# Kernel tuning notes

Measured on AMD Instinct MI355X. Metric: run time of the kernel, lower is better.

The kernel has to match this reference:

```python
import jax, jax.numpy as jnp
import numpy as np

EMBD_SIZE = 128
NUM_HEADS = 8
HEAD_SIZE = 16

def setup_inputs() -> dict:
    key = jax.random.key(0)
    ks = jax.random.split(key, 6)
    B, S = 8, 2048
    x = jax.random.normal(ks[0], (B, S, EMBD_SIZE), dtype=jnp.float32)
    # per-head Linear weights, torch layout [out, in] stacked over heads -> [H, hs, E]
    sc = 1.0 / np.sqrt(EMBD_SIZE)
    Wk = jax.random.normal(ks[1], (NUM_HEADS, HEAD_SIZE, EMBD_SIZE), dtype=jnp.float32) * sc
    Wq = jax.random.normal(ks[2], (NUM_HEADS, HEAD_SIZE, EMBD_SIZE), dtype=jnp.float32) * sc
    Wv = jax.random.normal(ks[3], (NUM_HEADS, HEAD_SIZE, EMBD_SIZE), dtype=jnp.float32) * sc
    Wp = jax.random.normal(ks[4], (EMBD_SIZE, NUM_HEADS * HEAD_SIZE), dtype=jnp.float32) * sc
    bp = jax.random.normal(ks[5], (EMBD_SIZE,), dtype=jnp.float32) * 0.01
    return {"x": x, "Wk": Wk, "Wq": Wq, "Wv": Wv, "Wp": Wp, "bp": bp}

def reference(x, Wk, Wq, Wv, Wp, bp):
    # x: [B,S,E]; W{k,q,v}: [H,hs,E]; Wp: [E,H*hs]
    B, S, E = x.shape
    H, hs, _ = Wk.shape
    q = jnp.einsum('bse,hde->bhsd', x, Wq)
    k = jnp.einsum('bse,hde->bhsd', x, Wk)
    v = jnp.einsum('bse,hde->bhsd', x, Wv)
    # NOTE: original code MULTIPLIES by sqrt(head_size) (k.shape[-1]**0.5)
    scores = jnp.einsum('bhsd,bhtd->bhst', q, k) * (hs ** 0.5)
    wei = jax.nn.softmax(scores, axis=-1)  # dropout is identity in eval mode
    out = jnp.einsum('bhst,bhtd->bhsd', wei, v)
    # concat heads along last dim: [B,S,H*hs]
    out = out.transpose(0, 2, 1, 3).reshape(B, S, H * hs)
    return out @ Wp.T + bp
```

## Files before the change

### kernel.cpp

```cpp
#include <hip/hip_runtime.h>
#include <hip/hip_bf16.h>

constexpr int Bb  = 8;
constexpr int Ss  = 2048;
constexpr int Ee  = 128;
constexpr int Hh  = 8;
constexpr int HSs = 16;
constexpr int QKVSZ = Bb * Hh * Ss * HSs;

typedef _Float16 f16;
typedef __attribute__((ext_vector_type(8)))  _Float16 f16x8;
typedef __attribute__((ext_vector_type(16))) float f32x16;

constexpr float QSCALE = 5.770780163555854f;

__device__ __forceinline__ unsigned pack_rtz(float lo, float hi) {
    union { __fp16 __attribute__((ext_vector_type(2))) h; unsigned u; } c;
    c.h = __builtin_amdgcn_cvt_pkrtz(lo, hi);
    return c.u;
}
__device__ __forceinline__ unsigned pack_rne(float lo, float hi) {
    union { __attribute__((ext_vector_type(2))) _Float16 h; unsigned u; } c;
    c.h[0] = (f16)lo; c.h[1] = (f16)hi;
    return c.u;
}

__device__ __forceinline__ float vmax16(const f32x16& v) {
    float a = fmaxf(fmaxf(v[0],  v[1]),  v[2]);
    float b = fmaxf(fmaxf(v[3],  v[4]),  v[5]);
    float c = fmaxf(fmaxf(v[6],  v[7]),  v[8]);
    float d = fmaxf(fmaxf(v[9],  v[10]), v[11]);
    float e = fmaxf(fmaxf(v[12], v[13]), v[14]);
    float g = fmaxf(fmaxf(a, b), c);
    float h = fmaxf(fmaxf(d, e), v[15]);
    return fmaxf(g, h);
}

__device__ __forceinline__ f16x8 cvt8(const float4& w0, const float4& w1) {
    union { f16x8 v; unsigned u[4]; } wf;
    wf.u[0] = pack_rne(w0.x, w0.y); wf.u[1] = pack_rne(w0.z, w0.w);
    wf.u[2] = pack_rne(w1.x, w1.y); wf.u[3] = pack_rne(w1.z, w1.w);
    return wf.v;
}

__global__ __launch_bounds__(256) void qkv_kernel(
    const float* __restrict__ x,
    const float* __restrict__ Wq, const float* __restrict__ Wk,
    const float* __restrict__ Wv,
    f16* __restrict__ qo, f16* __restrict__ ko, f16* __restrict__ vo)
{
    constexpr int LDW = 136;
    __shared__ __align__(16) f16 Xs[32 * LDW];

    const int rowbase = blockIdx.x * 32;

    for (int idx = threadIdx.x; idx < 32 * 32; idx += 256) {
        const int r = idx >> 5, cp = idx & 31;
        float4 v = *(const float4*)(x + (size_t)(rowbase + r) * Ee + cp * 4);
        union { f16 h[4]; uint2 u; } cv;
        cv.h[0] = (f16)v.x; cv.h[1] = (f16)v.y; cv.h[2] = (f16)v.z; cv.h[3] = (f16)v.w;
        *(uint2*)&Xs[r * LDW + cp * 4] = cv.u;
    }
    __syncthreads();

    const int wv_ = threadIdx.x >> 6, lane = threadIdx.x & 63;
    const int h = lane >> 5, n31 = lane & 31;

    f16x8 A[8];
#pragma unroll
    for (int t = 0; t < 8; ++t)
        A[t] = *(const f16x8*)&Xs[n31 * LDW + 16 * t + 8 * h];

    const int c = wv_ * 32 + n31;
    const int b = rowbase >> 11;
    const int s0 = rowbase & 2047;
    const int head = c >> 4, d = c & 15;
    const int bh = b * Hh + head;
    const int it = s0 >> 6, g0 = (s0 >> 4) & 3;

#pragma unroll
    for (int mat = 0; mat < 3; ++mat) {
        const float* W = (mat == 0) ? Wq : (mat == 1) ? Wk : Wv;
        const float* wr32 = W + (size_t)c * Ee + 8 * h;
        f32x16 acc = {};
#pragma unroll
        for (int t = 0; t < 8; ++t) {
            float4 w0 = *(const float4*)(wr32 + 16 * t);
            float4 w1 = *(const float4*)(wr32 + 16 * t + 4);
            acc = __builtin_amdgcn_mfma_f32_32x32x16_f16(A[t], cvt8(w0, w1), acc, 0, 0, 0);
        }

        if (mat < 2) {
            f16* dst = (mat == 0) ? qo : ko;
            const float scale = (mat == 1) ? QSCALE : 1.f;
#pragma unroll
            for (int r = 0; r < 16; ++r) {
                const int s = s0 + (r & 3) + 8 * (r >> 2) + 4 * h;
                dst[((size_t)bh * Ss + s) * HSs + d] = (f16)(acc[r] * scale);
            }
        } else {
            f16* vb = vo + (size_t)bh * 65536 + it * 2048;
#pragma unroll
            for (int rq = 0; rq < 4; ++rq) {
                union { f16 hv[4]; uint2 u; } pk4;
#pragma unroll
                for (int i = 0; i < 4; ++i) pk4.hv[i] = (f16)acc[4 * rq + i];
                *(uint2*)(vb + (g0 + (rq >> 1)) * 512 + (d + 32 * h) * 8 + 4 * (rq & 1)) = pk4.u;
            }
        }
    }

    for (int i = threadIdx.x; i < 512; i += 256) {
        const int gp = i >> 8, hd = (i >> 5) & 7, cc = i & 31;
        const int lanep = (cc < 16) ? 16 + cc : 32 + cc;
        const unsigned one2 = 0x3C003C00u;
        uint4 val = ((cc & 15) == 0) ? (uint4){one2, one2, one2, one2}
                                     : (uint4){0, 0, 0, 0};
        *(uint4*)(vo + (size_t)(b * Hh + hd) * 65536 + it * 2048
                  + (g0 + gp) * 512 + lanep * 8) = val;
    }
}

__global__ __launch_bounds__(512, 4) void attn_kernel(
    const f16* __restrict__ qg, const f16* __restrict__ kg,
    const f16* __restrict__ vg, const float* __restrict__ wp32,
    const float* __restrict__ bp, float* __restrict__ out)
{
    constexpr int LDW = 136;
    __shared__ __align__(16) f16 Os[32 * LDW];

    const int b    = blockIdx.x & 7;
    const int qblk = blockIdx.x >> 3;
    const int wid  = threadIdx.x >> 6;
    const int lane = threadIdx.x & 63;
    const int h    = lane >> 5;
    const int q31  = lane & 31;
    const int qbase = qblk * 32;
    const int bh   = b * Hh + wid;

    const f16x8 qf = *(const f16x8*)(qg + ((size_t)bh * Ss + qbase + q31) * HSs + 8 * h);

    const f16* pk = kg + (size_t)bh * Ss * HSs + q31 * 16 + 8 * h;
    const f16* pv = vg + (size_t)bh * 65536 + lane * 8;

    f16x8 ka0 = *(const f16x8*)pk;
    f16x8 ka1 = *(const f16x8*)(pk + 512);
    f16x8 va0 = *(const f16x8*)(pv);
    f16x8 va1 = *(const f16x8*)(pv + 512);
    f16x8 va2 = *(const f16x8*)(pv + 1024);
    f16x8 va3 = *(const f16x8*)(pv + 1536);

    f32x16 acc = {};
    f32x16 cinit = {};

    constexpr int NIT = Ss / 64;
    for (int it = 0; it < NIT; ++it) {
        f32x16 st0 = __builtin_amdgcn_mfma_f32_32x32x16_f16(ka0, qf, cinit, 0, 0, 0);
        f32x16 st1 = __builtin_amdgcn_mfma_f32_32x32x16_f16(ka1, qf, cinit, 0, 0, 0);

        if (it + 1 < NIT) {
            pk += 1024;
            ka0 = *(const f16x8*)pk;
            ka1 = *(const f16x8*)(pk + 512);
        }

        float mx = fmaxf(vmax16(st0), vmax16(st1));
        mx = fmaxf(mx, __shfl_xor(mx, 32, 64));

        if (__any(mx > 8.f)) {
            const float delta = fmaxf(mx, 0.f);
            const float corr  = __builtin_amdgcn_exp2f(-delta);
#pragma unroll
            for (int r = 0; r < 9; ++r) acc[r] *= corr;
#pragma unroll
            for (int t = 0; t < 16; ++t) { st0[t] -= delta; st1[t] -= delta; }
#pragma unroll
            for (int r = 0; r < 16; ++r) cinit[r] -= delta;
        }

        union { unsigned u[4]; f16x8 v; } B1, B2, B3, B4;
#pragma unroll
        for (int r = 0; r < 4; ++r) {
            B1.u[r] = pack_rtz(__builtin_amdgcn_exp2f(st0[2 * r]),
                               __builtin_amdgcn_exp2f(st0[2 * r + 1]));
            B2.u[r] = pack_rtz(__builtin_amdgcn_exp2f(st0[8 + 2 * r]),
                               __builtin_amdgcn_exp2f(st0[9 + 2 * r]));
            B3.u[r] = pack_rtz(__builtin_amdgcn_exp2f(st1[2 * r]),
                               __builtin_amdgcn_exp2f(st1[2 * r + 1]));
            B4.u[r] = pack_rtz(__builtin_amdgcn_exp2f(st1[8 + 2 * r]),
                               __builtin_amdgcn_exp2f(st1[9 + 2 * r]));
        }

        acc = __builtin_amdgcn_mfma_f32_32x32x16_f16(va0, B1.v, acc, 0, 0, 0);
        acc = __builtin_amdgcn_mfma_f32_32x32x16_f16(va1, B2.v, acc, 0, 0, 0);
        acc = __builtin_amdgcn_mfma_f32_32x32x16_f16(va2, B3.v, acc, 0, 0, 0);
        acc = __builtin_amdgcn_mfma_f32_32x32x16_f16(va3, B4.v, acc, 0, 0, 0);

        if (it + 1 < NIT) {
            pv += 2048;
            va0 = *(const f16x8*)(pv);
            va1 = *(const f16x8*)(pv + 512);
            va2 = *(const f16x8*)(pv + 1024);
            va3 = *(const f16x8*)(pv + 1536);
        }
    }

    const float l = acc[8] + __shfl_xor(acc[8], 32, 64);
    const float inv = 1.f / l;

    f16* orow = &Os[q31 * LDW + wid * HSs + 4 * h];
    uint2 lo = { pack_rne(acc[0] * inv, acc[1] * inv), pack_rne(acc[2] * inv, acc[3] * inv) };
    uint2 hi = { pack_rne(acc[4] * inv, acc[5] * inv), pack_rne(acc[6] * inv, acc[7] * inv) };
    *(uint2*)(orow)     = lo;
    *(uint2*)(orow + 8) = hi;
    __syncthreads();

    if (wid >= 4) return;

    f16x8 A[8];
#pragma unroll
    for (int t = 0; t < 8; ++t)
        A[t] = *(const f16x8*)&Os[q31 * LDW + 16 * t + 8 * h];

    const int e = wid * 32 + q31;
    const float* wr32 = wp32 + (size_t)e * Ee + 8 * h;
    f32x16 acc2 = {};
#pragma unroll
    for (int t = 0; t < 8; ++t) {
        float4 w0 = *(const float4*)(wr32 + 16 * t);
        float4 w1 = *(const float4*)(wr32 + 16 * t + 4);
        acc2 = __builtin_amdgcn_mfma_f32_32x32x16_f16(A[t], cvt8(w0, w1), acc2, 0, 0, 0);
    }

    const float bias = bp[e];
#pragma unroll
    for (int r = 0; r < 16; ++r) {
        const int R = qbase + (r & 3) + 8 * (r >> 2) + 4 * h;
        out[((size_t)b * Ss + R) * Ee + e] = acc2[r] + bias;
    }
}

extern "C" void kernel_launch(void* const* d_in, const int* in_sizes, int n_in,
                              void* d_out, int out_size, void* d_ws, size_t ws_size,
                              hipStream_t stream)
{
    const float* x  = (const float*)d_in[0];
    const float* Wk = (const float*)d_in[1];
    const float* Wq = (const float*)d_in[2];
    const float* Wv = (const float*)d_in[3];
    const float* Wp = (const float*)d_in[4];
    const float* bp = (const float*)d_in[5];
    float* out = (float*)d_out;

    f16* ws = (f16*)d_ws;
    f16* qh = ws;
    f16* kh = ws + (size_t)QKVSZ;
    f16* vh = ws + (size_t)2 * QKVSZ;

    qkv_kernel<<<Bb * Ss / 32, 256, 0, stream>>>(x, Wq, Wk, Wv, qh, kh, vh);
    attn_kernel<<<Bb * Ss / 32, 512, 0, stream>>>(qh, kh, vh, Wp, bp, out);
}
```

Measured before the change: 133.9 us.

## Split QKV projection across 8 waves and raise MFMA priority in attention

The QKV kernel now launches 512 threads. Four waves compute Q and K with swapped MFMA operands, which lets them write packed 4-element stores instead of scalar stores. The other four waves compute V and write the V padding pattern. This spreads the projection work across more waves and coalesces the Q/K writes. Separately, the PV MFMA block in the attention loop is wrapped in s_setprio to favour matrix-issue over other waves, which may help or hurt overlap with the softmax math.

```diff
diff --git a/kernel.cpp b/kernel.cpp
--- a/kernel.cpp
+++ b/kernel.cpp
@@ -43,7 +43,7 @@
     return wf.v;
 }
 
-__global__ __launch_bounds__(256) void qkv_kernel(
+__global__ __launch_bounds__(512, 4) void qkv_kernel(
     const float* __restrict__ x,
     const float* __restrict__ Wq, const float* __restrict__ Wk,
     const float* __restrict__ Wv,
@@ -54,7 +54,7 @@
 
     const int rowbase = blockIdx.x * 32;
 
-    for (int idx = threadIdx.x; idx < 32 * 32; idx += 256) {
+    for (int idx = threadIdx.x; idx < 32 * 32; idx += 512) {
         const int r = idx >> 5, cp = idx & 31;
         float4 v = *(const float4*)(x + (size_t)(rowbase + r) * Ee + cp * 4);
         union { f16 h[4]; uint2 u; } cv;
@@ -63,61 +63,74 @@
     }
     __syncthreads();
 
-    const int wv_ = threadIdx.x >> 6, lane = threadIdx.x & 63;
+    const int wid = threadIdx.x >> 6, lane = threadIdx.x & 63;
     const int h = lane >> 5, n31 = lane & 31;
 
-    f16x8 A[8];
+    f16x8 Xf[8];
 #pragma unroll
     for (int t = 0; t < 8; ++t)
-        A[t] = *(const f16x8*)&Xs[n31 * LDW + 16 * t + 8 * h];
-
-    const int c = wv_ * 32 + n31;
+        Xf[t] = *(const f16x8*)&Xs[n31 * LDW + 16 * t + 8 * h];
+
     const int b = rowbase >> 11;
     const int s0 = rowbase & 2047;
-    const int head = c >> 4, d = c & 15;
-    const int bh = b * Hh + head;
-    const int it = s0 >> 6, g0 = (s0 >> 4) & 3;
-
-#pragma unroll
-    for (int mat = 0; mat < 3; ++mat) {
-        const float* W = (mat == 0) ? Wq : (mat == 1) ? Wk : Wv;
-        const float* wr32 = W + (size_t)c * Ee + 8 * h;
+
+    if (wid < 4) {
+        const int s = s0 + n31;
+#pragma unroll
+        for (int mat = 0; mat < 2; ++mat) {
+            const float* W = (mat == 0) ? Wq : Wk;
+            const float* wr32 = W + (size_t)(wid * 32 + n31) * Ee + 8 * h;
+            f32x16 acc = {};
+#pragma unroll
+            for (int t = 0; t < 8; ++t) {
+                float4 w0 = *(const float4*)(wr32 + 16 * t);
+                float4 w1 = *(const float4*)(wr32 + 16 * t + 4);
+                acc = __builtin_amdgcn_mfma_f32_32x32x16_f16(cvt8(w0, w1), Xf[t], acc, 0, 0, 0);
+            }
+            f16* dst = (mat == 0) ? qo : ko;
+            const float scale = (mat == 1) ? QSCALE : 1.f;
+#pragma unroll
+            for (int rq = 0; rq < 4; ++rq) {
+                const int cbase = wid * 32 + 8 * rq + 4 * h;
+                const int head = cbase >> 4, dbase = cbase & 15;
+                union { f16 hv[4]; uint2 u; } pk4;
+#pragma unroll
+                for (int i = 0; i < 4; ++i) pk4.hv[i] = (f16)(acc[4 * rq + i] * scale);
+                *(uint2*)(dst + ((size_t)(b * Hh + head) * Ss + s) * HSs + dbase) = pk4.u;
+            }
+        }
+    } else {
+        const int g = wid - 4;
+        const int c = g * 32 + n31;
+        const int head = c >> 4, d = c & 15;
+        const int bh = b * Hh + head;
+        const int it = s0 >> 6, g0 = (s0 >> 4) & 3;
+        const float* wr32 = Wv + (size_t)c * Ee + 8 * h;
         f32x16 acc = {};
 #pragma unroll
         for (int t = 0; t < 8; ++t) {
             float4 w0 = *(const float4*)(wr32 + 16 * t);
             float4 w1 = *(const float4*)(wr32 + 16 * t + 4);
-            acc = __builtin_amdgcn_mfma_f32_32x32x16_f16(A[t], cvt8(w0, w1), acc, 0, 0, 0);
-        }
-
-        if (mat < 2) {
-            f16* dst = (mat == 0) ? qo : ko;
-            const float scale = (mat == 1) ? QSCALE : 1.f;
-#pragma unroll
-            for (int r = 0; r < 16; ++r) {
-                const int s = s0 + (r & 3) + 8 * (r >> 2) + 4 * h;
-                dst[((size_t)bh * Ss + s) * HSs + d] = (f16)(acc[r] * scale);
-            }
-        } else {
-            f16* vb = vo + (size_t)bh * 65536 + it * 2048;
-#pragma unroll
-            for (int rq = 0; rq < 4; ++rq) {
-                union { f16 hv[4]; uint2 u; } pk4;
-#pragma unroll
-                for (int i = 0; i < 4; ++i) pk4.hv[i] = (f16)acc[4 * rq + i];
-                *(uint2*)(vb + (g0 + (rq >> 1)) * 512 + (d + 32 * h) * 8 + 4 * (rq & 1)) = pk4.u;
-            }
-        }
-    }
-
-    for (int i = threadIdx.x; i < 512; i += 256) {
-        const int gp = i >> 8, hd = (i >> 5) & 7, cc = i & 31;
-        const int lanep = (cc < 16) ? 16 + cc : 32 + cc;
-        const unsigned one2 = 0x3C003C00u;
-        uint4 val = ((cc & 15) == 0) ? (uint4){one2, one2, one2, one2}
-                                     : (uint4){0, 0, 0, 0};
-        *(uint4*)(vo + (size_t)(b * Hh + hd) * 65536 + it * 2048
-                  + (g0 + gp) * 512 + lanep * 8) = val;
+            acc = __builtin_amdgcn_mfma_f32_32x32x16_f16(Xf[t], cvt8(w0, w1), acc, 0, 0, 0);
+        }
+        f16* vb = vo + (size_t)bh * 65536 + it * 2048;
+#pragma unroll
+        for (int rq = 0; rq < 4; ++rq) {
+            union { f16 hv[4]; uint2 u; } pk4;
+#pragma unroll
+            for (int i = 0; i < 4; ++i) pk4.hv[i] = (f16)acc[4 * rq + i];
+            *(uint2*)(vb + (g0 + (rq >> 1)) * 512 + (d + 32 * h) * 8 + 4 * (rq & 1)) = pk4.u;
+        }
+
+        for (int i = threadIdx.x - 256; i < 512; i += 256) {
+            const int gp = i >> 8, hd = (i >> 5) & 7, cc = i & 31;
+            const int lanep = (cc < 16) ? 16 + cc : 32 + cc;
+            const unsigned one2 = 0x3C003C00u;
+            uint4 val = ((cc & 15) == 0) ? (uint4){one2, one2, one2, one2}
+                                         : (uint4){0, 0, 0, 0};
+            *(uint4*)(vo + (size_t)(b * Hh + hd) * 65536 + it * 2048
+                      + (g0 + gp) * 512 + lanep * 8) = val;
+        }
     }
 }
 
@@ -191,10 +204,12 @@
                                __builtin_amdgcn_exp2f(st1[9 + 2 * r]));
         }
 
+        __builtin_amdgcn_s_setprio(1);
         acc = __builtin_amdgcn_mfma_f32_32x32x16_f16(va0, B1.v, acc, 0, 0, 0);
         acc = __builtin_amdgcn_mfma_f32_32x32x16_f16(va1, B2.v, acc, 0, 0, 0);
         acc = __builtin_amdgcn_mfma_f32_32x32x16_f16(va2, B3.v, acc, 0, 0, 0);
         acc = __builtin_amdgcn_mfma_f32_32x32x16_f16(va3, B4.v, acc, 0, 0, 0);
+        __builtin_amdgcn_s_setprio(0);
 
         if (it + 1 < NIT) {
             pv += 2048;
@@ -257,6 +272,6 @@
     f16* kh = ws + (size_t)QKVSZ;
     f16* vh = ws + (size_t)2 * QKVSZ;
 
-    qkv_kernel<<<Bb * Ss / 32, 256, 0, stream>>>(x, Wq, Wk, Wv, qh, kh, vh);
+    qkv_kernel<<<Bb * Ss / 32, 512, 0, stream>>>(x, Wq, Wk, Wv, qh, kh, vh);
     attn_kernel<<<Bb * Ss / 32, 512, 0, stream>>>(qh, kh, vh, Wp, bp, out);
 }
```

Measured after the change: 132.9 us. Within noise of the previous version (-0.7%).
